# Optimization experiments

Measured on AMD Instinct MI355X. Metric: run time of the kernel, lower is better.

## Reference

```python
import jax, jax.numpy as jnp
import numpy as np
from jax import lax

BN_EPS = 1e-5


def _conv_bn_relu(x, W, b, gamma, beta):
    # x: [B, Cin, N]; W: [Cout, Cin]; 1x1 conv == channel GEMM
    y = jnp.einsum('oc,bcn->bon', W, x) + b[None, :, None]
    mean = jnp.mean(y, axis=(0, 2), keepdims=True)
    var = jnp.mean((y - mean) ** 2, axis=(0, 2), keepdims=True)  # biased, torch BN train mode
    y = gamma[None, :, None] * (y - mean) / jnp.sqrt(var + BN_EPS) + beta[None, :, None]
    return jax.nn.relu(y)


def setup_inputs() -> dict:
    key = jax.random.key(0)
    ks = jax.random.split(key, 8)
    B, N1, N2, C1, C2 = 16, 4096, 1024, 128, 256
    Cin, H = C1 + C2, 256  # MLP dims [384, 256, 256]
    inp = {
        'centroids1': jax.random.normal(ks[0], (B, 3, N1), jnp.float32),
        'centroids2': jax.random.normal(ks[1], (B, 3, N2), jnp.float32),
        'features1': jax.random.normal(ks[2], (B, C1, N1), jnp.float32),
        'features2': jax.random.normal(ks[3], (B, C2, N2), jnp.float32),
        'W1': jax.random.normal(ks[4], (H, Cin), jnp.float32) / np.sqrt(Cin),
        'b1': jnp.zeros((H,), jnp.float32),
        'g1': jnp.ones((H,), jnp.float32),
        'be1': jnp.zeros((H,), jnp.float32),
        'W2': jax.random.normal(ks[5], (H, H), jnp.float32) / np.sqrt(H),
        'b2': jnp.zeros((H,), jnp.float32),
        'g2': jnp.ones((H,), jnp.float32),
        'be2': jnp.zeros((H,), jnp.float32),
    }
    return inp


def reference(centroids1, centroids2, features1, features2,
              W1, b1, g1, be1, W2, b2, g2, be2):
    c1 = centroids1.transpose(0, 2, 1)  # [B, N1, 3]
    c2 = centroids2.transpose(0, 2, 1)  # [B, N2, 3]
    f2 = features2.transpose(0, 2, 1)   # [B, N2, C2]

    # pairwise squared distances [B, N1, N2]
    d = (jnp.sum(c1 ** 2, -1)[:, :, None] + jnp.sum(c2 ** 2, -1)[:, None, :]
         - 2.0 * jnp.einsum('bnd,bmd->bnm', c1, c2))

    # 3 nearest neighbors (smallest distances)
    neg_top, idx = lax.top_k(-d, 3)            # idx: [B, N1, 3]
    dist3 = -neg_top
    recip = 1.0 / (dist3 + 1e-8)
    weight = recip / jnp.sum(recip, axis=2, keepdims=True)  # [B, N1, 3]

    gathered = jax.vmap(lambda f, i: f[i])(f2, idx)         # [B, N1, 3, C2]
    interp = jnp.sum(gathered * weight[..., None], axis=2)  # [B, N1, C2]

    feats = jnp.concatenate((features1.transpose(0, 2, 1), interp), axis=-1)  # [B, N1, C1+C2]
    x = feats.transpose(0, 2, 1)  # [B, C1+C2, N1]
    x = _conv_bn_relu(x, W1, b1, g1, be1)
    x = _conv_bn_relu(x, W2, b2, g2, be2)
    return x  # [B, 256, N1]
```

## Files before the change

### kernel.cpp

```cpp
#include <hip/hip_runtime.h>
#include <math.h>

#define N1 4096
#define N2 1024
#define C1 128
#define C2 256
#define CIN 384
#define H 256
#define BATCH 16
#define BN_EPS 1e-5f

typedef __attribute__((ext_vector_type(8))) short bf16x8;
typedef __attribute__((ext_vector_type(4))) float f32x4;

__device__ inline float bf2f(short s) {
    union { unsigned u; float f; } x;
    x.u = ((unsigned)(unsigned short)s) << 16;
    return x.f;
}
__device__ inline short f2bf(float f) {
    union { float f; unsigned u; } x; x.f = f;
    unsigned r = x.u + 0x7fffu + ((x.u >> 16) & 1u);
    return (short)(r >> 16);
}

typedef const __attribute__((address_space(1))) unsigned int guint;
typedef __attribute__((address_space(3))) unsigned int luint;
__device__ inline void gll16(const void* g, void* l) {
    __builtin_amdgcn_global_load_lds((guint*)g, (luint*)l, 16, 0, 0);
}

__global__ __launch_bounds__(512)
void prep_fused(const float* __restrict__ c1, const float* __restrict__ c2,
                const float* __restrict__ f2, const float* __restrict__ W1,
                const float* __restrict__ W2,
                float4* __restrict__ pk, short* __restrict__ f2t,
                short* __restrict__ W1s, short* __restrict__ W2s) {
    __shared__ __align__(16) char lds_raw[29184];
    const int blk = blockIdx.x;
    const int t = threadIdx.x;

    if (blk < 1024) {
        float4* sc = (float4*)lds_raw;
        float*  md = (float*)(lds_raw + 16384);
        int*    mi = (int*)(lds_raw + 16384 + 6400);
        const int b = blk >> 6, ng = blk & 63;
        const float* c2b = c2 + (size_t)b * 3 * N2;
        for (int j = t; j < N2; j += 512) {
            float xx = c2b[j], yy = c2b[N2 + j], zz = c2b[2 * N2 + j];
            sc[j] = make_float4(-2.f * xx, -2.f * yy, -2.f * zz, xx * xx + yy * yy + zz * zz);
        }
        __syncthreads();

        const int q = t & 63;
        const int oct = t >> 6;
        const int n = ng * 64 + q;
        const float* c1b = c1 + (size_t)b * 3 * N1;
        const float x = c1b[n], y = c1b[N1 + n], z = c1b[2 * N1 + n];

        float d0 = 3.4e38f, d1 = 3.4e38f, d2 = 3.4e38f;
        int i0 = 0, i1 = 0, i2 = 0;
        const int j0 = oct * 128;
        #pragma unroll 8
        for (int jj = 0; jj < 128; ++jj) {
            const int j = j0 + jj;
            float4 cc = sc[j];
            float d = fmaf(x, cc.x, fmaf(y, cc.y, fmaf(z, cc.z, cc.w)));
            bool c0v = d < d0, c1v = d < d1, c2v = d < d2;
            i2 = c1v ? i1 : (c2v ? j : i2);
            i1 = c0v ? i0 : (c1v ? j : i1);
            i0 = c0v ? j  : i0;
            d2 = __builtin_amdgcn_fmed3f(d1, d2, d);
            d1 = __builtin_amdgcn_fmed3f(d0, d1, d);
            d0 = fminf(d0, d);
        }
        const int mb = q * 25 + oct * 3;
        md[mb + 0] = d0; md[mb + 1] = d1; md[mb + 2] = d2;
        mi[mb + 0] = i0; mi[mb + 1] = i1; mi[mb + 2] = i2;
        __syncthreads();

        if (t < 64) {
            float e0 = 3.4e38f, e1 = 3.4e38f, e2 = 3.4e38f;
            int a0 = 0, a1 = 0, a2 = 0;
            #pragma unroll
            for (int r = 0; r < 24; ++r) {
                const int rr = t * 25 + r;
                float d = md[rr]; int j = mi[rr];
                bool c0 = d < e0, c1v = d < e1, c2v = d < e2;
                e2 = c1v ? e1 : (c2v ? d : e2);  a2 = c1v ? a1 : (c2v ? j : a2);
                e1 = c0 ? e0 : (c1v ? d : e1);   a1 = c0 ? a0 : (c1v ? j : a1);
                e0 = c0 ? d  : e0;               a0 = c0 ? j  : a0;
            }
            const float s1 = x * x + y * y + z * z;
            float r0 = 1.0f / (e0 + s1 + 1e-8f);
            float r1 = 1.0f / (e1 + s1 + 1e-8f);
            float r2 = 1.0f / (e2 + s1 + 1e-8f);
            float rs = r0 + r1 + r2;
            unsigned pack = (unsigned)a0 | ((unsigned)a1 << 10) | ((unsigned)a2 << 20);
            pk[(size_t)b * N1 + n] = make_float4(__uint_as_float(pack), r0 / rs, r1 / rs, r2 / rs);
        }
    } else if (blk < 3072) {
        typedef float (*st_t)[32][33];
        st_t st = (st_t)lds_raw;
        const int half = t >> 8, tt = t & 255;
        const int tid = (blk - 1024) * 2 + half;
        const int j0 = (tid & 31) * 32, c0 = ((tid >> 5) & 7) * 32, b = tid >> 8;
        {
            const int cc = tt >> 3, jj = (tt & 7) * 4;
            const float* src = f2 + ((size_t)b * C2 + c0 + cc) * N2 + j0 + jj;
            float4 v = *(const float4*)src;
            st[half][cc][jj + 0] = v.x; st[half][cc][jj + 1] = v.y;
            st[half][cc][jj + 2] = v.z; st[half][cc][jj + 3] = v.w;
        }
        __syncthreads();
        {
            const int j = tt >> 3, cb = (tt & 7) * 4;
            short4 v = { f2bf(st[half][cb + 0][j]), f2bf(st[half][cb + 1][j]),
                         f2bf(st[half][cb + 2][j]), f2bf(st[half][cb + 3][j]) };
            *(short4*)(f2t + ((size_t)b * N2 + j0 + j) * C2 + c0 + cb) = v;
        }
    } else {
        const bool w1 = (blk < 3096);
        const int K = w1 ? CIN : H;
        const int nkb = K >> 3;
        const int id = (blk - (w1 ? 3072 : 3096)) * 512 + t;
        if (id < 256 * nkb) {
            const float* W = w1 ? W1 : W2;
            short* Wsw = w1 ? W1s : W2s;
            const int m = id / nkb, kb = id % nkb;
            const float* src = W + (size_t)m * K + kb * 8;
            bf16x8 v;
            #pragma unroll
            for (int j = 0; j < 8; ++j) v[j] = f2bf(src[j]);
            *(bf16x8*)(Wsw + ((size_t)kb * 256 + m) * 8) = v;
        }
    }
}

template<int NT, bool BN>
__global__ __launch_bounds__(256)
void gemm_kernel(const short* __restrict__ Wsw,
                 const float* __restrict__ f1, const short* __restrict__ Bkc,
                 const short* __restrict__ f2t, const float4* __restrict__ pk,
                 const float* __restrict__ scale, const float* __restrict__ shift,
                 short* __restrict__ Ykc, float2* __restrict__ P) {
    constexpr bool M0 = (NT == 12);

    __shared__ __align__(16) short B_lds[4 * NT][64][8];
    __shared__ float sc_s[256], sh_s[256];

    const int t = threadIdx.x;
    const int blk = blockIdx.x;
    const int b = blk >> 6, nt = blk & 63;
    const int n0 = nt * 64;

    const int lane = t & 63, wv = t >> 6;
    const int wm = wv;
    const int l16 = lane & 15, lq = lane >> 4;

    if (BN) { sc_s[t] = scale[t]; sh_s[t] = shift[t]; }

    if (M0) {
        const int col = t & 63;
        const int kq  = t >> 6;
        float4 pv = pk[(size_t)b * N1 + n0 + col];
        unsigned u = __float_as_uint(pv.x);
        const short* rr0 = f2t + ((size_t)b * N2 + (u & 1023u)) * C2;
        const short* rr1 = f2t + ((size_t)b * N2 + ((u >> 10) & 1023u)) * C2;
        const short* rr2 = f2t + ((size_t)b * N2 + ((u >> 20) & 1023u)) * C2;
        #pragma unroll
        for (int i = 0; i < 8; ++i) {
            const int kbl = i * 4 + kq;
            bf16x8 g0 = *(const bf16x8*)(rr0 + kbl * 8);
            bf16x8 g1 = *(const bf16x8*)(rr1 + kbl * 8);
            bf16x8 g2 = *(const bf16x8*)(rr2 + kbl * 8);
            bf16x8 o;
            #pragma unroll
            for (int e = 0; e < 8; ++e)
                o[e] = f2bf(fmaf(pv.w, bf2f(g2[e]), fmaf(pv.z, bf2f(g1[e]), pv.y * bf2f(g0[e]))));
            *(bf16x8*)&B_lds[16 + kbl][col][0] = o;
        }
        const float* f1b = f1 + (size_t)b * C1 * N1;
        const int kbt = t >> 4, nq = (t & 15) * 4;
        float4 fv[8];
        #pragma unroll
        for (int e = 0; e < 8; ++e)
            fv[e] = *(const float4*)(f1b + (size_t)(kbt * 8 + e) * N1 + n0 + nq);
        #pragma unroll
        for (int j = 0; j < 4; ++j) {
            bf16x8 pw;
            pw[0] = f2bf(j == 0 ? fv[0].x : j == 1 ? fv[0].y : j == 2 ? fv[0].z : fv[0].w);
            pw[1] = f2bf(j == 0 ? fv[1].x : j == 1 ? fv[1].y : j == 2 ? fv[1].z : fv[1].w);
            pw[2] = f2bf(j == 0 ? fv[2].x : j == 1 ? fv[2].y : j == 2 ? fv[2].z : fv[2].w);
            pw[3] = f2bf(j == 0 ? fv[3].x : j == 1 ? fv[3].y : j == 2 ? fv[3].z : fv[3].w);
            pw[4] = f2bf(j == 0 ? fv[4].x : j == 1 ? fv[4].y : j == 2 ? fv[4].z : fv[4].w);
            pw[5] = f2bf(j == 0 ? fv[5].x : j == 1 ? fv[5].y : j == 2 ? fv[5].z : fv[5].w);
            pw[6] = f2bf(j == 0 ? fv[6].x : j == 1 ? fv[6].y : j == 2 ? fv[6].z : fv[6].w);
            pw[7] = f2bf(j == 0 ? fv[7].x : j == 1 ? fv[7].y : j == 2 ? fv[7].z : fv[7].w);
            *(bf16x8*)&B_lds[kbt][nq + j][0] = pw;
        }
    } else {
        const short* Bb = Bkc + (size_t)b * 32 * N1 * 8;
        #pragma unroll
        for (int i = 0; i < 8; ++i) {
            const int u = wv * 8 + i;
            const short* g = Bb + ((size_t)u * N1 + n0 + lane) * 8;
            gll16(g, &B_lds[u][0][0]);
        }
    }
    __syncthreads();

    f32x4 acc[4][4];
    #pragma unroll
    for (int i = 0; i < 4; ++i)
        #pragma unroll
        for (int j = 0; j < 4; ++j)
            acc[i][j] = (f32x4){0.f, 0.f, 0.f, 0.f};

    #pragma unroll
    for (int s = 0; s < NT; ++s) {
        bf16x8 a[4], bb4[4];
        const short* ap = Wsw + ((size_t)(s * 4 + lq) * 256 + wm * 64 + l16) * 8;
        #pragma unroll
        for (int f = 0; f < 4; ++f)
            a[f] = *(const bf16x8*)(ap + (size_t)f * 16 * 8);
        if (BN) {
            const int k0 = s * 32 + lq * 8;
            float sck[8], shk[8];
            #pragma unroll
            for (int e = 0; e < 8; ++e) { sck[e] = sc_s[k0 + e]; shk[e] = sh_s[k0 + e]; }
            #pragma unroll
            for (int f = 0; f < 4; ++f) {
                bf16x8 raw = *(const bf16x8*)&B_lds[s * 4 + lq][f * 16 + l16][0];
                #pragma unroll
                for (int e = 0; e < 8; ++e)
                    bb4[f][e] = f2bf(fmaxf(fmaf(bf2f(raw[e]), sck[e], shk[e]), 0.f));
            }
        } else {
            #pragma unroll
            for (int f = 0; f < 4; ++f)
                bb4[f] = *(const bf16x8*)&B_lds[s * 4 + lq][f * 16 + l16][0];
        }
        #pragma unroll
        for (int i = 0; i < 4; ++i)
            #pragma unroll
            for (int j = 0; j < 4; ++j)
                acc[i][j] = __builtin_amdgcn_mfma_f32_16x16x32_bf16(a[i], bb4[j], acc[i][j], 0, 0, 0);
    }

    short* Yb = Ykc + (size_t)b * 32 * N1 * 8;
    #pragma unroll
    for (int i = 0; i < 4; ++i) {
        const int kb = wm * 8 + i * 2 + (lq >> 1);
        const int kr0 = (lq & 1) * 4;
        #pragma unroll
        for (int j = 0; j < 4; ++j) {
            const int n = n0 + j * 16 + l16;
            short4 v = { f2bf(acc[i][j][0]), f2bf(acc[i][j][1]),
                         f2bf(acc[i][j][2]), f2bf(acc[i][j][3]) };
            *(short4*)(Yb + ((size_t)kb * N1 + n) * 8 + kr0) = v;
        }
    }

    #pragma unroll
    for (int i = 0; i < 4; ++i) {
        #pragma unroll
        for (int r = 0; r < 4; ++r) {
            float s = 0.f, qq = 0.f;
            #pragma unroll
            for (int j = 0; j < 4; ++j) {
                float xv = acc[i][j][r];
                s += xv; qq += xv * xv;
            }
            #pragma unroll
            for (int msk = 1; msk < 16; msk <<= 1) {
                s  += __shfl_xor(s, msk);
                qq += __shfl_xor(qq, msk);
            }
            if (l16 == 0) {
                const int c = wm * 64 + i * 16 + lq * 4 + r;
                P[(size_t)c * 1024 + blk] = make_float2(s, qq);
            }
        }
    }
}

__global__ __launch_bounds__(256)
void bn_reduce(const float2* __restrict__ P, const float* __restrict__ g,
               const float* __restrict__ be, float* __restrict__ scale,
               float* __restrict__ shift) {
    const int c = blockIdx.x, t = threadIdx.x;
    float s = 0.f, q = 0.f;
    #pragma unroll
    for (int r = 0; r < 4; ++r) {
        float2 v = P[(size_t)c * 1024 + r * 256 + t];
        s += v.x; q += v.y;
    }
    __shared__ float ss[256], sq[256];
    ss[t] = s; sq[t] = q;
    __syncthreads();
    for (int o = 128; o > 0; o >>= 1) {
        if (t < o) { ss[t] += ss[t + o]; sq[t] += sq[t + o]; }
        __syncthreads();
    }
    if (t == 0) {
        const float inv = 1.0f / (float)(BATCH * N1);
        float mean = ss[0] * inv;
        float var  = sq[0] * inv - mean * mean;
        float sc = g[c] / sqrtf(var + BN_EPS);
        scale[c] = sc;
        shift[c] = be[c] - mean * sc;
    }
}

__global__ __launch_bounds__(256)
void final_bn_relu(const short* __restrict__ y2kc, const float* __restrict__ scale,
                   const float* __restrict__ shift, float* __restrict__ out) {
    const int t = threadIdx.x;
    const int n0 = blockIdx.x * 1024 + t * 4;
    const int kb = blockIdx.y, b = blockIdx.z;
    const short* src = y2kc + ((size_t)(b * 32 + kb) * N1 + n0) * 8;
    bf16x8 v0 = *(const bf16x8*)(src);
    bf16x8 v1 = *(const bf16x8*)(src + 8);
    bf16x8 v2 = *(const bf16x8*)(src + 16);
    bf16x8 v3 = *(const bf16x8*)(src + 24);
    #pragma unroll
    for (int e = 0; e < 8; ++e) {
        const float sc = scale[kb * 8 + e], sh = shift[kb * 8 + e];
        float4 o;
        o.x = fmaxf(fmaf(bf2f(v0[e]), sc, sh), 0.f);
        o.y = fmaxf(fmaf(bf2f(v1[e]), sc, sh), 0.f);
        o.z = fmaxf(fmaf(bf2f(v2[e]), sc, sh), 0.f);
        o.w = fmaxf(fmaf(bf2f(v3[e]), sc, sh), 0.f);
        *(float4*)(out + ((size_t)(b * 256 + kb * 8 + e) * N1) + n0) = o;
    }
}

extern "C" void kernel_launch(void* const* d_in, const int* in_sizes, int n_in,
                              void* d_out, int out_size, void* d_ws, size_t ws_size,
                              hipStream_t stream) {
    const float* c1  = (const float*)d_in[0];
    const float* c2  = (const float*)d_in[1];
    const float* f1  = (const float*)d_in[2];
    const float* f2  = (const float*)d_in[3];
    const float* W1  = (const float*)d_in[4];
    const float* g1  = (const float*)d_in[6];
    const float* be1 = (const float*)d_in[7];
    const float* W2  = (const float*)d_in[8];
    const float* g2  = (const float*)d_in[10];
    const float* be2 = (const float*)d_in[11];
    float* out = (float*)d_out;

    char* ws = (char*)d_ws;
    short*  y1kc = (short*)ws;
    short*  f2t  = (short*)(ws + (32u << 20));
    short*  y2kc = (short*)(ws + (32u << 20));
    short*  W1s  = (short*)(ws + (64u << 20));
    short*  W2s  = (short*)(ws + (64u << 20) + (256u << 10));
    float4* pk   = (float4*)(ws + (64u << 20) + (512u << 10));
    float2* P    = (float2*)(ws + (64u << 20) + (1536u << 10));
    float* scale1 = (float*)(ws + (64u << 20) + (3584u << 10));
    float* shift1 = scale1 + 256;
    float* scale2 = shift1 + 256;
    float* shift2 = scale2 + 256;

    prep_fused<<<3112, 512, 0, stream>>>(c1, c2, f2, W1, W2, pk, f2t, W1s, W2s);

    gemm_kernel<12, false><<<1024, 256, 0, stream>>>(
        W1s, f1, nullptr, f2t, pk, nullptr, nullptr, y1kc, P);
    bn_reduce<<<256, 256, 0, stream>>>(P, g1, be1, scale1, shift1);

    gemm_kernel<8, true><<<1024, 256, 0, stream>>>(
        W2s, nullptr, y1kc, nullptr, nullptr, scale1, shift1, y2kc, P);
    bn_reduce<<<256, 256, 0, stream>>>(P, g2, be2, scale2, shift2);

    final_bn_relu<<<dim3(N1 / 1024, 32, BATCH), 256, 0, stream>>>(y2kc, scale2, shift2, out);
}
```

Measured before the change: 128.3 us.

## Split GEMM kernels, double-buffer weight loads, halve GEMM2 tile width

Replaces the templated GEMM with two specialised kernels. The first issues the features1 global loads before the gather-interpolate work so their latency overlaps it. Both kernels prefetch the next K-step's weight fragments into a second register set while the current step's MFMAs run, and raise wave priority around the MFMA loop. GEMM2 now uses 32-column tiles across 2048 blocks instead of 64-column tiles across 1024, aiming for more parallelism and lower LDS use. The cost is more per-block partial statistics (a larger bn_reduce input) and more register pressure from the extra fragment buffer.

```diff
diff --git a/kernel.cpp b/kernel.cpp
--- a/kernel.cpp
+++ b/kernel.cpp
@@ -137,17 +137,12 @@
     }
 }
 
-template<int NT, bool BN>
 __global__ __launch_bounds__(256)
-void gemm_kernel(const short* __restrict__ Wsw,
-                 const float* __restrict__ f1, const short* __restrict__ Bkc,
-                 const short* __restrict__ f2t, const float4* __restrict__ pk,
-                 const float* __restrict__ scale, const float* __restrict__ shift,
-                 short* __restrict__ Ykc, float2* __restrict__ P) {
-    constexpr bool M0 = (NT == 12);
-
-    __shared__ __align__(16) short B_lds[4 * NT][64][8];
-    __shared__ float sc_s[256], sh_s[256];
+void gemm1_kernel(const short* __restrict__ Wsw,
+                  const float* __restrict__ f1,
+                  const short* __restrict__ f2t, const float4* __restrict__ pk,
+                  short* __restrict__ Ykc, float2* __restrict__ P) {
+    __shared__ __align__(16) short B_lds[48][64][8];
 
     const int t = threadIdx.x;
     const int blk = blockIdx.x;
@@ -158,9 +153,14 @@
     const int wm = wv;
     const int l16 = lane & 15, lq = lane >> 4;
 
-    if (BN) { sc_s[t] = scale[t]; sh_s[t] = shift[t]; }
-
-    if (M0) {
+    const float* f1b = f1 + (size_t)b * C1 * N1;
+    const int kbt = t >> 4, nq = (t & 15) * 4;
+    float4 fv[8];
+    #pragma unroll
+    for (int e = 0; e < 8; ++e)
+        fv[e] = *(const float4*)(f1b + (size_t)(kbt * 8 + e) * N1 + n0 + nq);
+
+    {
         const int col = t & 63;
         const int kq  = t >> 6;
         float4 pv = pk[(size_t)b * N1 + n0 + col];
@@ -180,33 +180,19 @@
                 o[e] = f2bf(fmaf(pv.w, bf2f(g2[e]), fmaf(pv.z, bf2f(g1[e]), pv.y * bf2f(g0[e]))));
             *(bf16x8*)&B_lds[16 + kbl][col][0] = o;
         }
-        const float* f1b = f1 + (size_t)b * C1 * N1;
-        const int kbt = t >> 4, nq = (t & 15) * 4;
-        float4 fv[8];
-        #pragma unroll
-        for (int e = 0; e < 8; ++e)
-            fv[e] = *(const float4*)(f1b + (size_t)(kbt * 8 + e) * N1 + n0 + nq);
-        #pragma unroll
-        for (int j = 0; j < 4; ++j) {
-            bf16x8 pw;
-            pw[0] = f2bf(j == 0 ? fv[0].x : j == 1 ? fv[0].y : j == 2 ? fv[0].z : fv[0].w);
-            pw[1] = f2bf(j == 0 ? fv[1].x : j == 1 ? fv[1].y : j == 2 ? fv[1].z : fv[1].w);
-            pw[2] = f2bf(j == 0 ? fv[2].x : j == 1 ? fv[2].y : j == 2 ? fv[2].z : fv[2].w);
-            pw[3] = f2bf(j == 0 ? fv[3].x : j == 1 ? fv[3].y : j == 2 ? fv[3].z : fv[3].w);
-            pw[4] = f2bf(j == 0 ? fv[4].x : j == 1 ? fv[4].y : j == 2 ? fv[4].z : fv[4].w);
-            pw[5] = f2bf(j == 0 ? fv[5].x : j == 1 ? fv[5].y : j == 2 ? fv[5].z : fv[5].w);
-            pw[6] = f2bf(j == 0 ? fv[6].x : j == 1 ? fv[6].y : j == 2 ? fv[6].z : fv[6].w);
-            pw[7] = f2bf(j == 0 ? fv[7].x : j == 1 ? fv[7].y : j == 2 ? fv[7].z : fv[7].w);
-            *(bf16x8*)&B_lds[kbt][nq + j][0] = pw;
-        }
-    } else {
-        const short* Bb = Bkc + (size_t)b * 32 * N1 * 8;
-        #pragma unroll
-        for (int i = 0; i < 8; ++i) {
-            const int u = wv * 8 + i;
-            const short* g = Bb + ((size_t)u * N1 + n0 + lane) * 8;
-            gll16(g, &B_lds[u][0][0]);
-        }
+    }
+    #pragma unroll
+    for (int j = 0; j < 4; ++j) {
+        bf16x8 pw;
+        pw[0] = f2bf(j == 0 ? fv[0].x : j == 1 ? fv[0].y : j == 2 ? fv[0].z : fv[0].w);
+        pw[1] = f2bf(j == 0 ? fv[1].x : j == 1 ? fv[1].y : j == 2 ? fv[1].z : fv[1].w);
+        pw[2] = f2bf(j == 0 ? fv[2].x : j == 1 ? fv[2].y : j == 2 ? fv[2].z : fv[2].w);
+        pw[3] = f2bf(j == 0 ? fv[3].x : j == 1 ? fv[3].y : j == 2 ? fv[3].z : fv[3].w);
+        pw[4] = f2bf(j == 0 ? fv[4].x : j == 1 ? fv[4].y : j == 2 ? fv[4].z : fv[4].w);
+        pw[5] = f2bf(j == 0 ? fv[5].x : j == 1 ? fv[5].y : j == 2 ? fv[5].z : fv[5].w);
+        pw[6] = f2bf(j == 0 ? fv[6].x : j == 1 ? fv[6].y : j == 2 ? fv[6].z : fv[6].w);
+        pw[7] = f2bf(j == 0 ? fv[7].x : j == 1 ? fv[7].y : j == 2 ? fv[7].z : fv[7].w);
+        *(bf16x8*)&B_lds[kbt][nq + j][0] = pw;
     }
     __syncthreads();
 
@@ -217,36 +203,30 @@
         for (int j = 0; j < 4; ++j)
             acc[i][j] = (f32x4){0.f, 0.f, 0.f, 0.f};
 
-    #pragma unroll
-    for (int s = 0; s < NT; ++s) {
-        bf16x8 a[4], bb4[4];
+    bf16x8 aA[4], aB[4];
+    auto loadA = [&](int s, bf16x8* dst) {
         const short* ap = Wsw + ((size_t)(s * 4 + lq) * 256 + wm * 64 + l16) * 8;
         #pragma unroll
+        for (int f = 0; f < 4; ++f) dst[f] = *(const bf16x8*)(ap + (size_t)f * 16 * 8);
+    };
+    loadA(0, aA);
+    __builtin_amdgcn_s_setprio(1);
+    #pragma unroll
+    for (int s = 0; s < 12; ++s) {
+        bf16x8* acur = (s & 1) ? aB : aA;
+        bf16x8* anxt = (s & 1) ? aA : aB;
+        if (s + 1 < 12) loadA(s + 1, anxt);
+        bf16x8 bb4[4];
+        #pragma unroll
         for (int f = 0; f < 4; ++f)
-            a[f] = *(const bf16x8*)(ap + (size_t)f * 16 * 8);
-        if (BN) {
-            const int k0 = s * 32 + lq * 8;
-            float sck[8], shk[8];
-            #pragma unroll
-            for (int e = 0; e < 8; ++e) { sck[e] = sc_s[k0 + e]; shk[e] = sh_s[k0 + e]; }
-            #pragma unroll
-            for (int f = 0; f < 4; ++f) {
-                bf16x8 raw = *(const bf16x8*)&B_lds[s * 4 + lq][f * 16 + l16][0];
-                #pragma unroll
-                for (int e = 0; e < 8; ++e)
-                    bb4[f][e] = f2bf(fmaxf(fmaf(bf2f(raw[e]), sck[e], shk[e]), 0.f));
-            }
-        } else {
-            #pragma unroll
-            for (int f = 0; f < 4; ++f)
-                bb4[f] = *(const bf16x8*)&B_lds[s * 4 + lq][f * 16 + l16][0];
-        }
+            bb4[f] = *(const bf16x8*)&B_lds[s * 4 + lq][f * 16 + l16][0];
         #pragma unroll
         for (int i = 0; i < 4; ++i)
             #pragma unroll
             for (int j = 0; j < 4; ++j)
-                acc[i][j] = __builtin_amdgcn_mfma_f32_16x16x32_bf16(a[i], bb4[j], acc[i][j], 0, 0, 0);
-    }
+                acc[i][j] = __builtin_amdgcn_mfma_f32_16x16x32_bf16(acur[i], bb4[j], acc[i][j], 0, 0, 0);
+    }
+    __builtin_amdgcn_s_setprio(0);
 
     short* Yb = Ykc + (size_t)b * 32 * N1 * 8;
     #pragma unroll
@@ -285,6 +265,103 @@
     }
 }
 
+__global__ __launch_bounds__(256)
+void gemm2_kernel(const short* __restrict__ Wsw, const short* __restrict__ y1kc,
+                  const float* __restrict__ scale, const float* __restrict__ shift,
+                  short* __restrict__ Ykc, float2* __restrict__ P) {
+    __shared__ __align__(16) short B_lds[32][32][8];
+    __shared__ float sc_s[256], sh_s[256];
+
+    const int t = threadIdx.x;
+    const int blk = blockIdx.x;
+    const int b = blk >> 7, nt = blk & 127;
+    const int n0 = nt * 32;
+
+    const int lane = t & 63, wv = t >> 6;
+    const int wm = wv;
+    const int l16 = lane & 15, lq = lane >> 4;
+
+    sc_s[t] = scale[t]; sh_s[t] = shift[t];
+
+    #pragma unroll
+    for (int i = 0; i < 4; ++i) {
+        const int u = wv * 4 + i;
+        const short* g = y1kc + (((size_t)b * 32 + u * 2 + (lane >> 5)) * N1 + n0 + (lane & 31)) * 8;
+        gll16(g, &B_lds[u * 2][0][0]);
+    }
+    __syncthreads();
+
+    f32x4 acc[4][2];
+    #pragma unroll
+    for (int i = 0; i < 4; ++i) {
+        acc[i][0] = (f32x4){0.f, 0.f, 0.f, 0.f};
+        acc[i][1] = (f32x4){0.f, 0.f, 0.f, 0.f};
+    }
+
+    bf16x8 aA[4], aB[4];
+    auto loadA = [&](int s, bf16x8* dst) {
+        const short* ap = Wsw + ((size_t)(s * 4 + lq) * 256 + wm * 64 + l16) * 8;
+        #pragma unroll
+        for (int f = 0; f < 4; ++f) dst[f] = *(const bf16x8*)(ap + (size_t)f * 16 * 8);
+    };
+    loadA(0, aA);
+    __builtin_amdgcn_s_setprio(1);
+    #pragma unroll
+    for (int s = 0; s < 8; ++s) {
+        bf16x8* acur = (s & 1) ? aB : aA;
+        bf16x8* anxt = (s & 1) ? aA : aB;
+        if (s + 1 < 8) loadA(s + 1, anxt);
+        const int k0 = s * 32 + lq * 8;
+        bf16x8 bb4[2];
+        #pragma unroll
+        for (int f = 0; f < 2; ++f) {
+            bf16x8 raw = *(const bf16x8*)&B_lds[s * 4 + lq][f * 16 + l16][0];
+            #pragma unroll
+            for (int e = 0; e < 8; ++e)
+                bb4[f][e] = f2bf(fmaxf(fmaf(bf2f(raw[e]), sc_s[k0 + e], sh_s[k0 + e]), 0.f));
+        }
+        #pragma unroll
+        for (int i = 0; i < 4; ++i) {
+            acc[i][0] = __builtin_amdgcn_mfma_f32_16x16x32_bf16(acur[i], bb4[0], acc[i][0], 0, 0, 0);
+            acc[i][1] = __builtin_amdgcn_mfma_f32_16x16x32_bf16(acur[i], bb4[1], acc[i][1], 0, 0, 0);
+        }
+    }
+    __builtin_amdgcn_s_setprio(0);
+
+    short* Yb = Ykc + (size_t)b * 32 * N1 * 8;
+    #pragma unroll
+    for (int i = 0; i < 4; ++i) {
+        const int kb = wm * 8 + i * 2 + (lq >> 1);
+        const int kr0 = (lq & 1) * 4;
+        #pragma unroll
+        for (int j = 0; j < 2; ++j) {
+            const int n = n0 + j * 16 + l16;
+            short4 v = { f2bf(acc[i][j][0]), f2bf(acc[i][j][1]),
+                         f2bf(acc[i][j][2]), f2bf(acc[i][j][3]) };
+            *(short4*)(Yb + ((size_t)kb * N1 + n) * 8 + kr0) = v;
+        }
+    }
+
+    #pragma unroll
+    for (int i = 0; i < 4; ++i) {
+        #pragma unroll
+        for (int r = 0; r < 4; ++r) {
+            float s = acc[i][0][r] + acc[i][1][r];
+            float qq = acc[i][0][r] * acc[i][0][r] + acc[i][1][r] * acc[i][1][r];
+            #pragma unroll
+            for (int msk = 1; msk < 16; msk <<= 1) {
+                s  += __shfl_xor(s, msk);
+                qq += __shfl_xor(qq, msk);
+            }
+            if (l16 == 0) {
+                const int c = wm * 64 + i * 16 + lq * 4 + r;
+                P[(size_t)c * 2048 + blk] = make_float2(s, qq);
+            }
+        }
+    }
+}
+
+template<int NP>
 __global__ __launch_bounds__(256)
 void bn_reduce(const float2* __restrict__ P, const float* __restrict__ g,
                const float* __restrict__ be, float* __restrict__ scale,
@@ -292,8 +369,8 @@
     const int c = blockIdx.x, t = threadIdx.x;
     float s = 0.f, q = 0.f;
     #pragma unroll
-    for (int r = 0; r < 4; ++r) {
-        float2 v = P[(size_t)c * 1024 + r * 256 + t];
+    for (int r = 0; r < NP / 256; ++r) {
+        float2 v = P[(size_t)c * NP + r * 256 + t];
         s += v.x; q += v.y;
     }
     __shared__ float ss[256], sq[256];
@@ -356,23 +433,22 @@
     short*  f2t  = (short*)(ws + (32u << 20));
     short*  y2kc = (short*)(ws + (32u << 20));
     short*  W1s  = (short*)(ws + (64u << 20));
-    short*  W2s  = (short*)(ws + (64u << 20) + (256u << 10));
+    short*  W2s  = (short*)(ws + (64u << 20) + (192u << 10));
     float4* pk   = (float4*)(ws + (64u << 20) + (512u << 10));
-    float2* P    = (float2*)(ws + (64u << 20) + (1536u << 10));
-    float* scale1 = (float*)(ws + (64u << 20) + (3584u << 10));
+    float2* P1   = (float2*)(ws + (64u << 20) + (1536u << 10));
+    float2* P2   = (float2*)(ws + (64u << 20) + (512u << 10));
+    float* scale1 = (float*)(ws + (64u << 20) + (4608u << 10));
     float* shift1 = scale1 + 256;
     float* scale2 = shift1 + 256;
     float* shift2 = scale2 + 256;
 
     prep_fused<<<3112, 512, 0, stream>>>(c1, c2, f2, W1, W2, pk, f2t, W1s, W2s);
 
-    gemm_kernel<12, false><<<1024, 256, 0, stream>>>(
-        W1s, f1, nullptr, f2t, pk, nullptr, nullptr, y1kc, P);
-    bn_reduce<<<256, 256, 0, stream>>>(P, g1, be1, scale1, shift1);
-
-    gemm_kernel<8, true><<<1024, 256, 0, stream>>>(
-        W2s, nullptr, y1kc, nullptr, nullptr, scale1, shift1, y2kc, P);
-    bn_reduce<<<256, 256, 0, stream>>>(P, g2, be2, scale2, shift2);
+    gemm1_kernel<<<1024, 256, 0, stream>>>(W1s, f1, f2t, pk, y1kc, P1);
+    bn_reduce<1024><<<256, 256, 0, stream>>>(P1, g1, be1, scale1, shift1);
+
+    gemm2_kernel<<<2048, 256, 0, stream>>>(W2s, y1kc, scale1, shift1, y2kc, P2);
+    bn_reduce<2048><<<256, 256, 0, stream>>>(P2, g2, be2, scale2, shift2);
 
     final_bn_relu<<<dim3(N1 / 1024, 32, BATCH), 256, 0, stream>>>(y2kc, scale2, shift2, out);
 }
```

Measured after the change: 128.5 us. About the same (+0.1%).
